# Performance work log

Hardware: AMD Instinct MI355X
Metric: run time of the kernel (lower is better)

## Reference

```python
import jax, jax.numpy as jnp
import numpy as np

N = 100000
E = 1600000
IN_F = 128
OUT_F = 128
EPS = 1e-12


def setup_inputs() -> dict:
    key = jax.random.key(0)
    k1, k2, k3, k4, k5, k6 = jax.random.split(key, 6)
    x = jax.random.normal(k1, (N, IN_F), dtype=jnp.float32)
    rows = jnp.sort(jax.random.randint(k2, (E,), 0, N, dtype=jnp.int32))
    cols = jax.random.randint(k3, (E,), 0, N, dtype=jnp.int32)
    vals = jax.random.uniform(k4, (E,), dtype=jnp.float32)
    # nn.Linear(2*in_features, out_features): W is [out, 2*in], b is [out]
    bound = 1.0 / np.sqrt(2 * IN_F)
    W = jax.random.uniform(k5, (OUT_F, 2 * IN_F), dtype=jnp.float32, minval=-bound, maxval=bound)
    b = jax.random.uniform(k6, (OUT_F,), dtype=jnp.float32, minval=-bound, maxval=bound)
    return {"x": x, "rows": rows, "cols": cols, "vals": vals, "W": W, "b": b}


def reference(x, rows, cols, vals, W, b):
    # spmm(adj, x): gather source-node features, scale by edge weight,
    # segment-sum into destination rows.
    gathered = vals[:, None] * x[cols]                      # [E, in]
    neighbor = jax.ops.segment_sum(gathered, rows, num_segments=N)  # [N, in]
    combined = jnp.concatenate([x, neighbor], axis=1)       # [N, 2*in]
    out = combined @ W.T + b                                # [N, out]
    # F.normalize(out, p=2, dim=1): divide by max(||row||_2, eps)
    norm = jnp.sqrt(jnp.sum(out * out, axis=1, keepdims=True))
    return out / jnp.maximum(norm, EPS)
```

## Files before the change

kernel.cpp:

```cpp
#include <hip/hip_runtime.h>
#include <hip/hip_bf16.h>


typedef __bf16 bf16x8_t __attribute__((ext_vector_type(8)));
typedef float f32x4_t __attribute__((ext_vector_type(4)));
typedef float f32x2_t __attribute__((ext_vector_type(2)));

__device__ __forceinline__ unsigned int f32_to_bf16(float f) {
    unsigned int u = __float_as_uint(f);
    unsigned int r = u + 0x7fffu + ((u >> 16) & 1u);
    return r >> 16;
}
__device__ __forceinline__ unsigned int pack2(float a, float b) {
    return f32_to_bf16(a) | (f32_to_bf16(b) << 16);
}
__device__ __forceinline__ float bflo(unsigned int p) { return __uint_as_float(p << 16); }
__device__ __forceinline__ float bfhi(unsigned int p) { return __uint_as_float(p & 0xffff0000u); }

__global__ void prep_kernel(const float* __restrict__ x, uint4* __restrict__ xb4,
                            const int* __restrict__ rows, int* __restrict__ row_ptr,
                            const float* __restrict__ W, uint4* __restrict__ Wf,
                            int Nn, int Ee, int xcast_blks, int rowptr_blks) {
    int blk = blockIdx.x;
    if (blk < xcast_blks) {
        int i = blk * 256 + threadIdx.x;
        if (i < Nn * 16) {
            const float4* xf = (const float4*)x;
            float4 f0 = xf[(size_t)i * 2];
            float4 f1 = xf[(size_t)i * 2 + 1];
            uint4 o;
            o.x = pack2(f0.x, f0.y); o.y = pack2(f0.z, f0.w);
            o.z = pack2(f1.x, f1.y); o.w = pack2(f1.z, f1.w);
            xb4[i] = o;
        }
    } else if (blk < xcast_blks + rowptr_blks) {
        int n = (blk - xcast_blks) * 256 + threadIdx.x;
        if (n <= Nn) {
            int lo = 0, hi = Ee;
            while (lo < hi) {
                int mid = (lo + hi) >> 1;
                if (rows[mid] < n) lo = mid + 1; else hi = mid;
            }
            row_ptr[n] = lo;
        }
    } else {
        int i = (blk - xcast_blks - rowptr_blks) * 256 + threadIdx.x;
        int lane = i & 63, ks = (i >> 6) & 7, t = i >> 9;
        int row = t * 16 + (lane & 15);
        int col = ks * 32 + (lane >> 4) * 8;
        const float* p = W + (size_t)row * 256 + col;
        uint4 o;
        o.x = pack2(p[0], p[1]); o.y = pack2(p[2], p[3]);
        o.z = pack2(p[4], p[5]); o.w = pack2(p[6], p[7]);
        Wf[i] = o;
    }
}

__global__ __launch_bounds__(256, 8) void agg_kernel(
        const int* __restrict__ row_ptr, const int* __restrict__ cols,
        const float* __restrict__ vals, const char* __restrict__ xb,
        uint4* __restrict__ nb, int Nn) {
    int lane = threadIdx.x & 63;
    int wave = threadIdx.x >> 6;
    int h = lane >> 4;
    int l = lane & 15;
    int n = (blockIdx.x * 4 + wave) * 4 + h;
    bool valid = n < Nn;
    int nn = valid ? n : Nn - 1;
    int start = row_ptr[nn], end = row_ptr[nn + 1];
    if (!valid) end = start;
    unsigned loff = (unsigned)l << 4;

    f32x2_t a0 = {0.f, 0.f}, a1 = {0.f, 0.f}, a2 = {0.f, 0.f}, a3 = {0.f, 0.f};

#define EDGE(E, C, V)                                              \
    {                                                              \
        int q = max(min((E), end - 1), 0);                         \
        C = cols[q];                                               \
        V = ((E) < end) ? vals[q] : 0.f;                           \
    }
#define ACC(P, V)                                                  \
    {                                                              \
        f32x2_t vv = {(V), (V)};                                   \
        f32x2_t t0 = {bflo((P).x), bfhi((P).x)};                   \
        f32x2_t t1 = {bflo((P).y), bfhi((P).y)};                   \
        f32x2_t t2 = {bflo((P).z), bfhi((P).z)};                   \
        f32x2_t t3 = {bflo((P).w), bfhi((P).w)};                   \
        a0 += vv * t0; a1 += vv * t1; a2 += vv * t2; a3 += vv * t3;\
    }

    int e = start;
    int c0 = 0, c1 = 0; float v0 = 0.f, v1 = 0.f;
    if (e < end) { EDGE(e, c0, v0); EDGE(e + 1, c1, v1); }
    while (e < end) {
        int e2 = e + 2;
        int d0 = 0, d1 = 0; float w0 = 0.f, w1 = 0.f;
        if (e2 < end) { EDGE(e2, d0, w0); EDGE(e2 + 1, d1, w1); }
        uint4 p0 = *(const uint4*)(xb + (((unsigned)c0 << 8) | loff));
        uint4 p1 = *(const uint4*)(xb + (((unsigned)c1 << 8) | loff));
        ACC(p0, v0);
        ACC(p1, v1);
        c0 = d0; v0 = w0; c1 = d1; v1 = w1;
        e = e2;
    }
#undef EDGE
#undef ACC

    if (valid) {
        uint4 o;
        o.x = pack2(a0.x, a0.y); o.y = pack2(a1.x, a1.y);
        o.z = pack2(a2.x, a2.y); o.w = pack2(a3.x, a3.y);
        nb[(size_t)n * 16 + l] = o;
    }
}

__global__ __launch_bounds__(256, 3) void gemm_norm_kernel(
        const unsigned short* __restrict__ xb, const unsigned short* __restrict__ nb,
        const bf16x8_t* __restrict__ Wf, const float* __restrict__ b,
        float* __restrict__ out, int Nn) {
    int lane = threadIdx.x & 63;
    int wave = threadIdx.x >> 6;
    int m    = lane & 15;
    int quad = lane >> 4;
    int r0   = (blockIdx.x * 4 + wave) * 32;

    int arow0 = min(r0 + m, Nn - 1);
    int arow1 = min(r0 + 16 + m, Nn - 1);
    const bf16x8_t* Ax0 = (const bf16x8_t*)(xb + (size_t)arow0 * 128);
    const bf16x8_t* An0 = (const bf16x8_t*)(nb + (size_t)arow0 * 128);
    const bf16x8_t* Ax1 = (const bf16x8_t*)(xb + (size_t)arow1 * 128);
    const bf16x8_t* An1 = (const bf16x8_t*)(nb + (size_t)arow1 * 128);

    bf16x8_t a0[8], a1[8];
#pragma unroll
    for (int ks = 0; ks < 4; ++ks) {
        a0[ks]     = Ax0[ks * 4 + quad];
        a0[4 + ks] = An0[ks * 4 + quad];
        a1[ks]     = Ax1[ks * 4 + quad];
        a1[4 + ks] = An1[ks * 4 + quad];
    }

    f32x4_t acc0[8], acc1[8];
#pragma unroll
    for (int t = 0; t < 8; ++t) {
        acc0[t] = (f32x4_t){0.f, 0.f, 0.f, 0.f};
        acc1[t] = (f32x4_t){0.f, 0.f, 0.f, 0.f};
    }

#pragma unroll
    for (int t = 0; t < 8; ++t) {
#pragma unroll
        for (int ks = 0; ks < 8; ++ks) {
            bf16x8_t B = Wf[(t * 8 + ks) * 64 + lane];
            acc0[t] = __builtin_amdgcn_mfma_f32_16x16x32_bf16(a0[ks], B, acc0[t], 0, 0, 0);
            acc1[t] = __builtin_amdgcn_mfma_f32_16x16x32_bf16(a1[ks], B, acc1[t], 0, 0, 0);
        }
    }

    float bc[8];
#pragma unroll
    for (int t = 0; t < 8; ++t) bc[t] = b[t * 16 + m];

    float sq0[4] = {0.f, 0.f, 0.f, 0.f}, sq1[4] = {0.f, 0.f, 0.f, 0.f};
#pragma unroll
    for (int t = 0; t < 8; ++t)
#pragma unroll
        for (int r = 0; r < 4; ++r) {
            float u0 = acc0[t][r] + bc[t];
            float u1 = acc1[t][r] + bc[t];
            sq0[r] += u0 * u0;
            sq1[r] += u1 * u1;
        }
#pragma unroll
    for (int off = 1; off <= 8; off <<= 1) {
#pragma unroll
        for (int r = 0; r < 4; ++r) {
            sq0[r] += __shfl_xor(sq0[r], off, 64);
            sq1[r] += __shfl_xor(sq1[r], off, 64);
        }
    }
    float sc0[4], sc1[4];
#pragma unroll
    for (int r = 0; r < 4; ++r) {
        sc0[r] = 1.f / fmaxf(sqrtf(sq0[r]), 1e-12f);
        sc1[r] = 1.f / fmaxf(sqrtf(sq1[r]), 1e-12f);
    }

#pragma unroll
    for (int r = 0; r < 4; ++r) {
        int row0 = r0 + quad * 4 + r;
        int row1 = r0 + 16 + quad * 4 + r;
        if (row0 < Nn) {
            float* orow = out + (size_t)row0 * 128;
#pragma unroll
            for (int t = 0; t < 8; ++t) orow[t * 16 + m] = (acc0[t][r] + bc[t]) * sc0[r];
        }
        if (row1 < Nn) {
            float* orow = out + (size_t)row1 * 128;
#pragma unroll
            for (int t = 0; t < 8; ++t) orow[t * 16 + m] = (acc1[t][r] + bc[t]) * sc1[r];
        }
    }
}

extern "C" void kernel_launch(void* const* d_in, const int* in_sizes, int n_in,
                              void* d_out, int out_size, void* d_ws, size_t ws_size,
                              hipStream_t stream) {
    const float* x    = (const float*)d_in[0];
    const int*   rows = (const int*)  d_in[1];
    const int*   cols = (const int*)  d_in[2];
    const float* vals = (const float*)d_in[3];
    const float* W    = (const float*)d_in[4];
    const float* b    = (const float*)d_in[5];
    float*       out  = (float*)d_out;

    const int Nn = in_sizes[0] / 128;
    const int Ee = in_sizes[1];

    char*  ws      = (char*)d_ws;
    int*   row_ptr = (int*)ws;
    uint4* Wf      = (uint4*)(ws + 448 * 1024);
    uint4* xb      = (uint4*)(ws + 640 * 1024);
    uint4* nb      = (uint4*)(ws + 640 * 1024 + (size_t)Nn * 256);

    const int xcast_blks  = (Nn * 16 + 255) / 256;
    const int rowptr_blks = (Nn + 1 + 255) / 256;
    const int wcast_blks  = 16;

    prep_kernel<<<xcast_blks + rowptr_blks + wcast_blks, 256, 0, stream>>>(
        x, xb, rows, row_ptr, W, Wf, Nn, Ee, xcast_blks, rowptr_blks);
    agg_kernel<<<(Nn + 15) / 16, 256, 0, stream>>>(
        row_ptr, cols, vals, (const char*)xb, nb, Nn);
    gemm_norm_kernel<<<(Nn + 127) / 128, 256, 0, stream>>>(
        (const unsigned short*)xb, (const unsigned short*)nb,
        (const bf16x8_t*)Wf, b, out, Nn);
}
```

Baseline: 214.5 us.

## Fuse aggregation and GEMM-normalize into one kernel via LDS staging

Merges the sparse aggregation and the GEMM+L2-normalize kernels into a single kernel. Each block aggregates 16 nodes into shared memory, then its four waves each compute two 16-column output tiles with MFMA and combine row norms through LDS. This removes the round trip of the neighbor matrix through global memory and one kernel launch. The gather loop also widens from two to four edges in flight. In exchange, W fragments are reloaded per 16-row block instead of per 128 rows, and the block adds two barriers.

```diff
diff --git a/kernel.cpp b/kernel.cpp
--- a/kernel.cpp
+++ b/kernel.cpp
@@ -56,149 +56,144 @@
     }
 }
 
-__global__ __launch_bounds__(256, 8) void agg_kernel(
-        const int* __restrict__ row_ptr, const int* __restrict__ cols,
-        const float* __restrict__ vals, const char* __restrict__ xb,
-        uint4* __restrict__ nb, int Nn) {
+__global__ void fused_kernel(const int* __restrict__ row_ptr,
+                             const int* __restrict__ cols,
+                             const float* __restrict__ vals,
+                             const char* __restrict__ xbB,
+                             const bf16x8_t* __restrict__ Wf,
+                             const float* __restrict__ b,
+                             float* __restrict__ out, int Nn) {
+    __shared__ uint4 nbLDS[16 * 17];
+    __shared__ float __attribute__((aligned(16))) sqLDS[16][4];
+
     int lane = threadIdx.x & 63;
-    int wave = threadIdx.x >> 6;
-    int h = lane >> 4;
-    int l = lane & 15;
-    int n = (blockIdx.x * 4 + wave) * 4 + h;
-    bool valid = n < Nn;
-    int nn = valid ? n : Nn - 1;
-    int start = row_ptr[nn], end = row_ptr[nn + 1];
-    if (!valid) end = start;
-    unsigned loff = (unsigned)l << 4;
-
-    f32x2_t a0 = {0.f, 0.f}, a1 = {0.f, 0.f}, a2 = {0.f, 0.f}, a3 = {0.f, 0.f};
-
-#define EDGE(E, C, V)                                              \
-    {                                                              \
-        int q = max(min((E), end - 1), 0);                         \
-        C = cols[q];                                               \
-        V = ((E) < end) ? vals[q] : 0.f;                           \
-    }
-#define ACC(P, V)                                                  \
-    {                                                              \
-        f32x2_t vv = {(V), (V)};                                   \
-        f32x2_t t0 = {bflo((P).x), bfhi((P).x)};                   \
-        f32x2_t t1 = {bflo((P).y), bfhi((P).y)};                   \
-        f32x2_t t2 = {bflo((P).z), bfhi((P).z)};                   \
-        f32x2_t t3 = {bflo((P).w), bfhi((P).w)};                   \
-        a0 += vv * t0; a1 += vv * t1; a2 += vv * t2; a3 += vv * t3;\
-    }
-
-    int e = start;
-    int c0 = 0, c1 = 0; float v0 = 0.f, v1 = 0.f;
-    if (e < end) { EDGE(e, c0, v0); EDGE(e + 1, c1, v1); }
-    while (e < end) {
-        int e2 = e + 2;
-        int d0 = 0, d1 = 0; float w0 = 0.f, w1 = 0.f;
-        if (e2 < end) { EDGE(e2, d0, w0); EDGE(e2 + 1, d1, w1); }
-        uint4 p0 = *(const uint4*)(xb + (((unsigned)c0 << 8) | loff));
-        uint4 p1 = *(const uint4*)(xb + (((unsigned)c1 << 8) | loff));
-        ACC(p0, v0);
-        ACC(p1, v1);
-        c0 = d0; v0 = w0; c1 = d1; v1 = w1;
-        e = e2;
-    }
-#undef EDGE
+    int w    = threadIdx.x >> 6;
+
+    {
+        int h = lane >> 4;
+        int l = lane & 15;
+        int node = w * 4 + h;
+        int n = blockIdx.x * 16 + node;
+        int nn = min(n, Nn - 1);
+        int start = row_ptr[nn], end = row_ptr[nn + 1];
+        if (n >= Nn) end = start;
+        unsigned loff = (unsigned)l << 4;
+
+        f32x2_t a0 = {0.f, 0.f}, a1 = {0.f, 0.f}, a2 = {0.f, 0.f}, a3 = {0.f, 0.f};
+
+#define EDGE4(E, C0, C1, C2, C3, V0, V1, V2, V3)                                \
+        {                                                                       \
+            int q0 = min((E), end - 1),     q1 = min((E) + 1, end - 1);         \
+            int q2 = min((E) + 2, end - 1), q3 = min((E) + 3, end - 1);         \
+            C0 = cols[q0]; C1 = cols[q1]; C2 = cols[q2]; C3 = cols[q3];         \
+            V0 = ((E)     < end) ? vals[q0] : 0.f;                              \
+            V1 = ((E) + 1 < end) ? vals[q1] : 0.f;                              \
+            V2 = ((E) + 2 < end) ? vals[q2] : 0.f;                              \
+            V3 = ((E) + 3 < end) ? vals[q3] : 0.f;                              \
+        }
+#define ACC(P, V)                                                               \
+        {                                                                       \
+            f32x2_t vv = {(V), (V)};                                            \
+            f32x2_t t0 = {bflo((P).x), bfhi((P).x)};                            \
+            f32x2_t t1 = {bflo((P).y), bfhi((P).y)};                            \
+            f32x2_t t2 = {bflo((P).z), bfhi((P).z)};                            \
+            f32x2_t t3 = {bflo((P).w), bfhi((P).w)};                            \
+            a0 += vv * t0; a1 += vv * t1; a2 += vv * t2; a3 += vv * t3;         \
+        }
+
+        int e = start;
+        int c0 = 0, c1 = 0, c2 = 0, c3 = 0;
+        float v0 = 0.f, v1 = 0.f, v2 = 0.f, v3 = 0.f;
+        if (e < end) EDGE4(e, c0, c1, c2, c3, v0, v1, v2, v3);
+        while (e < end) {
+            int en = e + 4;
+            int d0 = 0, d1 = 0, d2 = 0, d3 = 0;
+            float w0 = 0.f, w1 = 0.f, w2 = 0.f, w3 = 0.f;
+            if (en < end) EDGE4(en, d0, d1, d2, d3, w0, w1, w2, w3);
+            uint4 p0 = *(const uint4*)(xbB + (((unsigned)c0 << 8) | loff));
+            uint4 p1 = *(const uint4*)(xbB + (((unsigned)c1 << 8) | loff));
+            uint4 p2 = *(const uint4*)(xbB + (((unsigned)c2 << 8) | loff));
+            uint4 p3 = *(const uint4*)(xbB + (((unsigned)c3 << 8) | loff));
+            ACC(p0, v0); ACC(p1, v1); ACC(p2, v2); ACC(p3, v3);
+            c0 = d0; c1 = d1; c2 = d2; c3 = d3;
+            v0 = w0; v1 = w1; v2 = w2; v3 = w3;
+            e = en;
+        }
+#undef EDGE4
 #undef ACC
 
-    if (valid) {
         uint4 o;
         o.x = pack2(a0.x, a0.y); o.y = pack2(a1.x, a1.y);
         o.z = pack2(a2.x, a2.y); o.w = pack2(a3.x, a3.y);
-        nb[(size_t)n * 16 + l] = o;
-    }
-}
-
-__global__ __launch_bounds__(256, 3) void gemm_norm_kernel(
-        const unsigned short* __restrict__ xb, const unsigned short* __restrict__ nb,
-        const bf16x8_t* __restrict__ Wf, const float* __restrict__ b,
-        float* __restrict__ out, int Nn) {
-    int lane = threadIdx.x & 63;
-    int wave = threadIdx.x >> 6;
+        nbLDS[node * 17 + l] = o;
+    }
+    __syncthreads();
+
     int m    = lane & 15;
     int quad = lane >> 4;
-    int r0   = (blockIdx.x * 4 + wave) * 32;
-
-    int arow0 = min(r0 + m, Nn - 1);
-    int arow1 = min(r0 + 16 + m, Nn - 1);
-    const bf16x8_t* Ax0 = (const bf16x8_t*)(xb + (size_t)arow0 * 128);
-    const bf16x8_t* An0 = (const bf16x8_t*)(nb + (size_t)arow0 * 128);
-    const bf16x8_t* Ax1 = (const bf16x8_t*)(xb + (size_t)arow1 * 128);
-    const bf16x8_t* An1 = (const bf16x8_t*)(nb + (size_t)arow1 * 128);
-
-    bf16x8_t a0[8], a1[8];
-#pragma unroll
-    for (int ks = 0; ks < 4; ++ks) {
-        a0[ks]     = Ax0[ks * 4 + quad];
-        a0[4 + ks] = An0[ks * 4 + quad];
-        a1[ks]     = Ax1[ks * 4 + quad];
-        a1[4 + ks] = An1[ks * 4 + quad];
-    }
-
-    f32x4_t acc0[8], acc1[8];
-#pragma unroll
-    for (int t = 0; t < 8; ++t) {
-        acc0[t] = (f32x4_t){0.f, 0.f, 0.f, 0.f};
-        acc1[t] = (f32x4_t){0.f, 0.f, 0.f, 0.f};
-    }
-
-#pragma unroll
-    for (int t = 0; t < 8; ++t) {
+    int r0   = blockIdx.x * 16;
+
+    int arow = min(r0 + m, Nn - 1);
+    const bf16x8_t* Ax = (const bf16x8_t*)(xbB + (size_t)arow * 256);
+
+    bf16x8_t a[8];
+#pragma unroll
+    for (int ks = 0; ks < 4; ++ks) a[ks] = Ax[ks * 4 + quad];
+#pragma unroll
+    for (int ks = 0; ks < 4; ++ks)
+        a[4 + ks] = *(const bf16x8_t*)&nbLDS[m * 17 + ks * 4 + quad];
+
+    f32x4_t acc[2];
+    float bc[2];
+#pragma unroll
+    for (int j = 0; j < 2; ++j) {
+        int t = w * 2 + j;
+        acc[j] = (f32x4_t){0.f, 0.f, 0.f, 0.f};
+        bc[j]  = b[t * 16 + m];
 #pragma unroll
         for (int ks = 0; ks < 8; ++ks) {
-            bf16x8_t B = Wf[(t * 8 + ks) * 64 + lane];
-            acc0[t] = __builtin_amdgcn_mfma_f32_16x16x32_bf16(a0[ks], B, acc0[t], 0, 0, 0);
-            acc1[t] = __builtin_amdgcn_mfma_f32_16x16x32_bf16(a1[ks], B, acc1[t], 0, 0, 0);
-        }
-    }
-
-    float bc[8];
-#pragma unroll
-    for (int t = 0; t < 8; ++t) bc[t] = b[t * 16 + m];
-
-    float sq0[4] = {0.f, 0.f, 0.f, 0.f}, sq1[4] = {0.f, 0.f, 0.f, 0.f};
-#pragma unroll
-    for (int t = 0; t < 8; ++t)
+            acc[j] = __builtin_amdgcn_mfma_f32_16x16x32_bf16(
+                a[ks], Wf[(t * 8 + ks) * 64 + lane], acc[j], 0, 0, 0);
+        }
+    }
+
+    float sq[4] = {0.f, 0.f, 0.f, 0.f};
+#pragma unroll
+    for (int j = 0; j < 2; ++j)
 #pragma unroll
         for (int r = 0; r < 4; ++r) {
-            float u0 = acc0[t][r] + bc[t];
-            float u1 = acc1[t][r] + bc[t];
-            sq0[r] += u0 * u0;
-            sq1[r] += u1 * u1;
+            float u = acc[j][r] + bc[j];
+            sq[r] += u * u;
         }
 #pragma unroll
     for (int off = 1; off <= 8; off <<= 1) {
 #pragma unroll
-        for (int r = 0; r < 4; ++r) {
-            sq0[r] += __shfl_xor(sq0[r], off, 64);
-            sq1[r] += __shfl_xor(sq1[r], off, 64);
-        }
-    }
-    float sc0[4], sc1[4];
+        for (int r = 0; r < 4; ++r) sq[r] += __shfl_xor(sq[r], off, 64);
+    }
+    if (m == 0) {
+#pragma unroll
+        for (int r = 0; r < 4; ++r) sqLDS[quad * 4 + r][w] = sq[r];
+    }
+    __syncthreads();
+
+    float scale[4];
 #pragma unroll
     for (int r = 0; r < 4; ++r) {
-        sc0[r] = 1.f / fmaxf(sqrtf(sq0[r]), 1e-12f);
-        sc1[r] = 1.f / fmaxf(sqrtf(sq1[r]), 1e-12f);
+        const float4 q4 = *(const float4*)sqLDS[quad * 4 + r];
+        float tot = q4.x + q4.y + q4.z + q4.w;
+        scale[r] = 1.f / fmaxf(sqrtf(tot), 1e-12f);
     }
 
 #pragma unroll
     for (int r = 0; r < 4; ++r) {
-        int row0 = r0 + quad * 4 + r;
-        int row1 = r0 + 16 + quad * 4 + r;
-        if (row0 < Nn) {
-            float* orow = out + (size_t)row0 * 128;
-#pragma unroll
-            for (int t = 0; t < 8; ++t) orow[t * 16 + m] = (acc0[t][r] + bc[t]) * sc0[r];
-        }
-        if (row1 < Nn) {
-            float* orow = out + (size_t)row1 * 128;
-#pragma unroll
-            for (int t = 0; t < 8; ++t) orow[t * 16 + m] = (acc1[t][r] + bc[t]) * sc1[r];
+        int row = r0 + quad * 4 + r;
+        if (row < Nn) {
+            float* orow = out + (size_t)row * 128;
+#pragma unroll
+            for (int j = 0; j < 2; ++j) {
+                int t = w * 2 + j;
+                orow[t * 16 + m] = (acc[j][r] + bc[j]) * scale[r];
+            }
         }
     }
 }
@@ -221,7 +216,6 @@
     int*   row_ptr = (int*)ws;
     uint4* Wf      = (uint4*)(ws + 448 * 1024);
     uint4* xb      = (uint4*)(ws + 640 * 1024);
-    uint4* nb      = (uint4*)(ws + 640 * 1024 + (size_t)Nn * 256);
 
     const int xcast_blks  = (Nn * 16 + 255) / 256;
     const int rowptr_blks = (Nn + 1 + 255) / 256;
@@ -229,9 +223,7 @@
 
     prep_kernel<<<xcast_blks + rowptr_blks + wcast_blks, 256, 0, stream>>>(
         x, xb, rows, row_ptr, W, Wf, Nn, Ee, xcast_blks, rowptr_blks);
-    agg_kernel<<<(Nn + 15) / 16, 256, 0, stream>>>(
-        row_ptr, cols, vals, (const char*)xb, nb, Nn);
-    gemm_norm_kernel<<<(Nn + 127) / 128, 256, 0, stream>>>(
-        (const unsigned short*)xb, (const unsigned short*)nb,
+    fused_kernel<<<(Nn + 15) / 16, 256, 0, stream>>>(
+        row_ptr, cols, vals, (const char*)xb,
         (const bf16x8_t*)Wf, b, out, Nn);
 }
```

New measurement: 197.0 us. 8.2% less time.
